# Kernel tuning notes

Measured on AMD Instinct MI355X. Metric: run time of the kernel, lower is better.

The kernel has to match this reference:

```python
import jax, jax.numpy as jnp
import numpy as np

B, T, D, H, O = 1024, 2048, 13, 128, 2


def setup_inputs() -> dict:
    key = jax.random.key(0)
    k1, k2, k3, k4 = jax.random.split(key, 4)
    xs = jax.random.normal(k1, (B, T, D), dtype=jnp.float32)
    # nn.Linear(in, out, bias=False) weights: [out, in]
    W_in = jax.random.normal(k2, (H, D), dtype=jnp.float32) / np.sqrt(D).astype(np.float32)
    W_h = jax.random.normal(k3, (H, H), dtype=jnp.float32) / np.sqrt(H).astype(np.float32)
    W_out = jax.random.normal(k4, (O, H), dtype=jnp.float32) / np.sqrt(H).astype(np.float32)
    return {"xs": xs, "W_in": W_in, "W_h": W_h, "W_out": W_out}


def reference(xs, W_in, W_h, W_out):
    # Vanilla hardtanh RNN, h0 = 0 (first step y = hardtanh(in_h(x)) == hardtanh(in_h(x) + W_h @ 0)).
    # Precompute all input projections in one big GEMM: [B, T, H]
    pre = jnp.einsum('btd,hd->bth', xs, W_in)

    def step(h, xh_t):  # h: [B, H], xh_t: [B, H]
        h = jnp.clip(xh_t + h @ W_h.T, -1.0, 1.0)  # F.hardtanh
        return h, None

    h0 = jnp.zeros((xs.shape[0], W_in.shape[0]), dtype=xs.dtype)
    hT, _ = jax.lax.scan(step, h0, jnp.swapaxes(pre, 0, 1))  # scan over time
    # Only the final hidden state per sequence is projected to the output.
    return hT @ W_out.T  # [B, O]
```

## Files before the change

kernel.cpp:

```cpp
#include <hip/hip_runtime.h>
#include <stdint.h>


#define RNN_B 1024
#define RNN_T 2048
#define RNN_D 13
#define RNN_H 128
#define RNN_O 2

#define NB 16
#define NWAVE 4
#define NTHR (NWAVE * 64)
#define ROWS 136

using f32x4 = __attribute__((ext_vector_type(4))) float;
using v8s   = __attribute__((ext_vector_type(8))) short;

__device__ __forceinline__ short f2bf(float f) {
    union { float f; uint32_t u; } c; c.f = f;
    uint32_t u = c.u + 0x7fffu + ((c.u >> 16) & 1u);
    return (short)(u >> 16);
}
__device__ __forceinline__ float bf2fs(short s) {
    union { uint32_t u; float f; } c; c.u = ((uint32_t)(uint16_t)s) << 16;
    return c.f;
}
__device__ __forceinline__ float bitf(uint32_t u) {
    union { uint32_t u; float f; } c; c.u = u; return c.f;
}
__device__ __forceinline__ uint32_t cvtpk(float a, float b) {
    uint32_t r;
    asm("v_cvt_pk_bf16_f32 %0, %1, %2" : "=v"(r) : "v"(a), "v"(b));
    return r;
}
__device__ __forceinline__ v8s pack4(uint32_t a, uint32_t b, uint32_t c, uint32_t d) {
    union { uint32_t u[4]; v8s s; } z;
    z.u[0] = a; z.u[1] = b; z.u[2] = c; z.u[3] = d; return z.s;
}
__device__ __forceinline__ float clamp1(float v) {
    return __builtin_amdgcn_fmed3f(v, -1.0f, 1.0f);
}

__device__ __forceinline__ void barrier_lgkm() {
    __builtin_amdgcn_sched_barrier(0);
    asm volatile("s_waitcnt lgkmcnt(0)" ::: "memory");
    __builtin_amdgcn_s_barrier();
    asm volatile("" ::: "memory");
    __builtin_amdgcn_sched_barrier(0);
}

#define STEP(CUR, NXT, X0, X1, X2, X3, TPF)                                      \
  do {                                                                           \
    v8s bh[4], bl[4];                                                            \
    bh[0] = *(const v8s*)&Hhi[CUR][n][g8];                                       \
    bh[1] = *(const v8s*)&Hhi[CUR][n][32 + g8];                                  \
    bh[2] = *(const v8s*)&Hhi[CUR][n][64 + g8];                                  \
    bh[3] = *(const v8s*)&Hhi[CUR][n][96 + g8];                                  \
    bl[0] = *(const v8s*)&Hlo[CUR][n][g8];                                       \
    bl[1] = *(const v8s*)&Hlo[CUR][n][32 + g8];                                  \
    bl[2] = *(const v8s*)&Hlo[CUR][n][64 + g8];                                  \
    bl[3] = *(const v8s*)&Hlo[CUR][n][96 + g8];                                  \
    float m0 = X0, m1 = X1, m2 = X2, m3 = X3;                                    \
    if (g == 3) { m1 = 0.0f; m2 = 0.0f; m3 = 0.0f; }                             \
    uint32_t xh01 = cvtpk(m0, m1), xh23 = cvtpk(m2, m3);                         \
    float q0 = m0 - bitf(xh01 << 16);                                            \
    float q1 = m1 - bitf(xh01 & 0xffff0000u);                                    \
    float q2 = m2 - bitf(xh23 << 16);                                            \
    float q3 = m3 - bitf(xh23 & 0xffff0000u);                                    \
    uint32_t xl01 = cvtpk(q0, q1), xl23 = cvtpk(q2, q3);                         \
    v8s xh = pack4(xh01, xh23, 0u, 0u);                                          \
    v8s xl = pack4(xl01, xl23, 0u, 0u);                                          \
    if ((TPF) < RNN_T) {                                                         \
      const float* xp = xrow + (size_t)(TPF) * RNN_D;                            \
      X0 = xp[d0]; X1 = xp[d1]; X2 = xp[d2]; X3 = xp[d3];                        \
    }                                                                            \
    f32x4 A1 = {0.f,0.f,0.f,0.f};                                                \
    f32x4 A2 = A1, A3 = A1, B1 = A1, B2 = A1, B3 = A1;                           \
    _Pragma("unroll")                                                            \
    for (int kt = 0; kt < 4; ++kt) {                                             \
      A1 = __builtin_amdgcn_mfma_f32_16x16x32_bf16(whiA[kt], bh[kt], A1, 0,0,0); \
      B1 = __builtin_amdgcn_mfma_f32_16x16x32_bf16(whiB[kt], bh[kt], B1, 0,0,0); \
      A2 = __builtin_amdgcn_mfma_f32_16x16x32_bf16(whiA[kt], bl[kt], A2, 0,0,0); \
      B2 = __builtin_amdgcn_mfma_f32_16x16x32_bf16(whiB[kt], bl[kt], B2, 0,0,0); \
      A3 = __builtin_amdgcn_mfma_f32_16x16x32_bf16(wloA[kt], bh[kt], A3, 0,0,0); \
      B3 = __builtin_amdgcn_mfma_f32_16x16x32_bf16(wloB[kt], bh[kt], B3, 0,0,0); \
    }                                                                            \
    A1 = __builtin_amdgcn_mfma_f32_16x16x32_bf16(whiA[4], xh, A1, 0,0,0);        \
    B1 = __builtin_amdgcn_mfma_f32_16x16x32_bf16(whiB[4], xh, B1, 0,0,0);        \
    A2 = __builtin_amdgcn_mfma_f32_16x16x32_bf16(whiA[4], xl, A2, 0,0,0);        \
    B2 = __builtin_amdgcn_mfma_f32_16x16x32_bf16(whiB[4], xl, B2, 0,0,0);        \
    A3 = __builtin_amdgcn_mfma_f32_16x16x32_bf16(wloA[4], xh, A3, 0,0,0);        \
    B3 = __builtin_amdgcn_mfma_f32_16x16x32_bf16(wloB[4], xh, B3, 0,0,0);        \
    {                                                                            \
      float v0 = clamp1(A1[0] + A2[0] + A3[0]);                                  \
      float v1 = clamp1(A1[1] + A2[1] + A3[1]);                                  \
      float v2 = clamp1(A1[2] + A2[2] + A3[2]);                                  \
      float v3 = clamp1(A1[3] + A2[3] + A3[3]);                                  \
      uint32_t h01 = cvtpk(v0, v1), h23 = cvtpk(v2, v3);                         \
      float p0 = v0 - bitf(h01 << 16);                                           \
      float p1 = v1 - bitf(h01 & 0xffff0000u);                                   \
      float p2 = v2 - bitf(h23 << 16);                                           \
      float p3 = v3 - bitf(h23 & 0xffff0000u);                                   \
      uint32_t l01 = cvtpk(p0, p1), l23 = cvtpk(p2, p3);                         \
      int2 wv; wv.x = (int)h01; wv.y = (int)h23;                                 \
      *(int2*)&Hhi[NXT][n][wbase + g8] = wv;                                     \
      wv.x = (int)l01; wv.y = (int)l23;                                          \
      *(int2*)&Hlo[NXT][n][wbase + g8] = wv;                                     \
    }                                                                            \
    {                                                                            \
      float v0 = clamp1(B1[0] + B2[0] + B3[0]);                                  \
      float v1 = clamp1(B1[1] + B2[1] + B3[1]);                                  \
      float v2 = clamp1(B1[2] + B2[2] + B3[2]);                                  \
      float v3 = clamp1(B1[3] + B2[3] + B3[3]);                                  \
      uint32_t h01 = cvtpk(v0, v1), h23 = cvtpk(v2, v3);                         \
      float p0 = v0 - bitf(h01 << 16);                                           \
      float p1 = v1 - bitf(h01 & 0xffff0000u);                                   \
      float p2 = v2 - bitf(h23 << 16);                                           \
      float p3 = v3 - bitf(h23 & 0xffff0000u);                                   \
      uint32_t l01 = cvtpk(p0, p1), l23 = cvtpk(p2, p3);                         \
      int2 wv; wv.x = (int)h01; wv.y = (int)h23;                                 \
      *(int2*)&Hhi[NXT][n][wbase + g8 + 4] = wv;                                 \
      wv.x = (int)l01; wv.y = (int)l23;                                          \
      *(int2*)&Hlo[NXT][n][wbase + g8 + 4] = wv;                                 \
    }                                                                            \
    barrier_lgkm();                                                              \
  } while (0)

__global__ __launch_bounds__(NTHR, 1) void rnn_mfma8_kernel(
    const float* __restrict__ xs,
    const float* __restrict__ W_in,
    const float* __restrict__ W_h,
    const float* __restrict__ W_out,
    float* __restrict__ out)
{
    __shared__ __align__(16) short Hhi[2][NB][ROWS];
    __shared__ __align__(16) short Hlo[2][NB][ROWS];

    const int tid  = threadIdx.x;
    const int lane = tid & 63;
    const int wid  = tid >> 6;
    const int n    = lane & 15;
    const int g    = lane >> 4;
    const int g8   = g * 8;
    const int wbase = 32 * wid;
    const int b0   = blockIdx.x * NB;

    const int d0 = (4 * g + 0 > 12) ? 12 : 4 * g + 0;
    const int d1 = (4 * g + 1 > 12) ? 12 : 4 * g + 1;
    const int d2 = (4 * g + 2 > 12) ? 12 : 4 * g + 2;
    const int d3 = (4 * g + 3 > 12) ? 12 : 4 * g + 3;

    v8s whiA[5], wloA[5], whiB[5], wloB[5];
    #pragma unroll
    for (int mi = 0; mi < 2; ++mi) {
        const int row = 16 * (wid * 2 + mi) + n;
        #pragma unroll
        for (int kt = 0; kt < 5; ++kt) {
            v8s h8, l8;
            #pragma unroll
            for (int j = 0; j < 4; ++j) {
                float w1, w2;
                if (kt < 4) {
                    w1 = W_h[row * RNN_H + 32 * kt + 4 * g + j];
                    w2 = W_h[row * RNN_H + 32 * kt + 16 + 4 * g + j];
                } else {
                    const int kx = 4 * g + j;
                    w1 = (kx < RNN_D) ? W_in[row * RNN_D + kx] : 0.0f;
                    w2 = 0.0f;
                }
                const short h1 = f2bf(w1);
                const short h2 = f2bf(w2);
                h8[j] = h1; h8[4 + j] = h2;
                l8[j] = f2bf(w1 - bf2fs(h1));
                l8[4 + j] = f2bf(w2 - bf2fs(h2));
            }
            if (mi == 0) { whiA[kt] = h8; wloA[kt] = l8; }
            else         { whiB[kt] = h8; wloB[kt] = l8; }
        }
    }

    for (int idx = tid; idx < NB * ROWS; idx += NTHR) {
        (&Hhi[0][0][0])[idx] = 0;
        (&Hlo[0][0][0])[idx] = 0;
    }

    const float* xrow = xs + (size_t)(b0 + n) * RNN_T * RNN_D;
    float xa0 = xrow[d0], xa1 = xrow[d1], xa2 = xrow[d2], xa3 = xrow[d3];
    float xb0 = xrow[RNN_D + d0], xb1 = xrow[RNN_D + d1];
    float xb2 = xrow[RNN_D + d2], xb3 = xrow[RNN_D + d3];
    __syncthreads();

    for (int t = 0; t < RNN_T; t += 2) {
        STEP(0, 1, xa0, xa1, xa2, xa3, t + 2);
        STEP(1, 0, xb0, xb1, xb2, xb3, t + 3);
    }

    __syncthreads();

    if (wid == 0 && lane < NB * RNN_O) {
        const int nn = lane & 15;
        const int o  = lane >> 4;
        float acc = 0.0f;
        for (int i = 0; i < RNN_H; ++i) {
            const int pos = 32 * (i >> 5) + 8 * ((i >> 2) & 3)
                          + 4 * ((i >> 4) & 1) + (i & 3);
            const float hv = bf2fs(Hhi[0][nn][pos]) + bf2fs(Hlo[0][nn][pos]);
            acc = fmaf(W_out[o * RNN_H + i], hv, acc);
        }
        out[(size_t)(b0 + nn) * RNN_O + o] = acc;
    }
}

extern "C" void kernel_launch(void* const* d_in, const int* in_sizes, int n_in,
                              void* d_out, int out_size, void* d_ws, size_t ws_size,
                              hipStream_t stream) {
    const float* xs    = (const float*)d_in[0];
    const float* W_in  = (const float*)d_in[1];
    const float* W_h   = (const float*)d_in[2];
    const float* W_out = (const float*)d_in[3];
    float* out = (float*)d_out;

    rnn_mfma8_kernel<<<RNN_B / NB, NTHR, 0, stream>>>(xs, W_in, W_h, W_out, out);
}
```

Baseline: 1.248 ms.

## Process two 16-sequence groups per block and issue input MFMAs first

Each block now handles 32 sequences as two independent 16-sequence groups of four waves, each group with its own LDS hidden-state buffers, and all eight waves share one barrier. The input-projection MFMAs are issued at the start of each step from zero accumulators, ahead of the recurrent MFMAs, so they can overlap the LDS reads of the hidden state. The aim is to hide the latency of the step-to-step dependency chain by interleaving two groups on one CU. In exchange the grid halves, so fewer CUs are used and each CU carries twice the MFMA work per step.

```diff
diff --git a/kernel.cpp b/kernel.cpp
--- a/kernel.cpp
+++ b/kernel.cpp
@@ -8,8 +8,8 @@
 #define RNN_H 128
 #define RNN_O 2
 
-#define NB 16
-#define NWAVE 4
+#define NB 32
+#define NWAVE 8
 #define NTHR (NWAVE * 64)
 #define ROWS 136
 
@@ -51,15 +51,17 @@
 
 #define STEP(CUR, NXT, X0, X1, X2, X3, TPF)                                      \
   do {                                                                           \
+                              \
     v8s bh[4], bl[4];                                                            \
-    bh[0] = *(const v8s*)&Hhi[CUR][n][g8];                                       \
-    bh[1] = *(const v8s*)&Hhi[CUR][n][32 + g8];                                  \
-    bh[2] = *(const v8s*)&Hhi[CUR][n][64 + g8];                                  \
-    bh[3] = *(const v8s*)&Hhi[CUR][n][96 + g8];                                  \
-    bl[0] = *(const v8s*)&Hlo[CUR][n][g8];                                       \
-    bl[1] = *(const v8s*)&Hlo[CUR][n][32 + g8];                                  \
-    bl[2] = *(const v8s*)&Hlo[CUR][n][64 + g8];                                  \
-    bl[3] = *(const v8s*)&Hlo[CUR][n][96 + g8];                                  \
+    bh[0] = *(const v8s*)&Hhi[CUR][grp][n][g8];                                  \
+    bh[1] = *(const v8s*)&Hhi[CUR][grp][n][32 + g8];                             \
+    bh[2] = *(const v8s*)&Hhi[CUR][grp][n][64 + g8];                             \
+    bh[3] = *(const v8s*)&Hhi[CUR][grp][n][96 + g8];                             \
+    bl[0] = *(const v8s*)&Hlo[CUR][grp][n][g8];                                  \
+    bl[1] = *(const v8s*)&Hlo[CUR][grp][n][32 + g8];                             \
+    bl[2] = *(const v8s*)&Hlo[CUR][grp][n][64 + g8];                             \
+    bl[3] = *(const v8s*)&Hlo[CUR][grp][n][96 + g8];                             \
+                           \
     float m0 = X0, m1 = X1, m2 = X2, m3 = X3;                                    \
     if (g == 3) { m1 = 0.0f; m2 = 0.0f; m3 = 0.0f; }                             \
     uint32_t xh01 = cvtpk(m0, m1), xh23 = cvtpk(m2, m3);                         \
@@ -70,12 +72,20 @@
     uint32_t xl01 = cvtpk(q0, q1), xl23 = cvtpk(q2, q3);                         \
     v8s xh = pack4(xh01, xh23, 0u, 0u);                                          \
     v8s xl = pack4(xl01, xl23, 0u, 0u);                                          \
+                  \
+    f32x4 Z = {0.f, 0.f, 0.f, 0.f};                                              \
+    f32x4 A1 = __builtin_amdgcn_mfma_f32_16x16x32_bf16(whiA[4], xh, Z, 0,0,0);   \
+    f32x4 B1 = __builtin_amdgcn_mfma_f32_16x16x32_bf16(whiB[4], xh, Z, 0,0,0);   \
+    f32x4 A2 = __builtin_amdgcn_mfma_f32_16x16x32_bf16(whiA[4], xl, Z, 0,0,0);   \
+    f32x4 B2 = __builtin_amdgcn_mfma_f32_16x16x32_bf16(whiB[4], xl, Z, 0,0,0);   \
+    f32x4 A3 = __builtin_amdgcn_mfma_f32_16x16x32_bf16(wloA[4], xh, Z, 0,0,0);   \
+    f32x4 B3 = __builtin_amdgcn_mfma_f32_16x16x32_bf16(wloB[4], xh, Z, 0,0,0);   \
+                                              \
     if ((TPF) < RNN_T) {                                                         \
       const float* xp = xrow + (size_t)(TPF) * RNN_D;                            \
       X0 = xp[d0]; X1 = xp[d1]; X2 = xp[d2]; X3 = xp[d3];                        \
     }                                                                            \
-    f32x4 A1 = {0.f,0.f,0.f,0.f};                                                \
-    f32x4 A2 = A1, A3 = A1, B1 = A1, B2 = A1, B3 = A1;                           \
+                                        \
     _Pragma("unroll")                                                            \
     for (int kt = 0; kt < 4; ++kt) {                                             \
       A1 = __builtin_amdgcn_mfma_f32_16x16x32_bf16(whiA[kt], bh[kt], A1, 0,0,0); \
@@ -85,12 +95,7 @@
       A3 = __builtin_amdgcn_mfma_f32_16x16x32_bf16(wloA[kt], bh[kt], A3, 0,0,0); \
       B3 = __builtin_amdgcn_mfma_f32_16x16x32_bf16(wloB[kt], bh[kt], B3, 0,0,0); \
     }                                                                            \
-    A1 = __builtin_amdgcn_mfma_f32_16x16x32_bf16(whiA[4], xh, A1, 0,0,0);        \
-    B1 = __builtin_amdgcn_mfma_f32_16x16x32_bf16(whiB[4], xh, B1, 0,0,0);        \
-    A2 = __builtin_amdgcn_mfma_f32_16x16x32_bf16(whiA[4], xl, A2, 0,0,0);        \
-    B2 = __builtin_amdgcn_mfma_f32_16x16x32_bf16(whiB[4], xl, B2, 0,0,0);        \
-    A3 = __builtin_amdgcn_mfma_f32_16x16x32_bf16(wloA[4], xh, A3, 0,0,0);        \
-    B3 = __builtin_amdgcn_mfma_f32_16x16x32_bf16(wloB[4], xh, B3, 0,0,0);        \
+                 \
     {                                                                            \
       float v0 = clamp1(A1[0] + A2[0] + A3[0]);                                  \
       float v1 = clamp1(A1[1] + A2[1] + A3[1]);                                  \
@@ -103,9 +108,9 @@
       float p3 = v3 - bitf(h23 & 0xffff0000u);                                   \
       uint32_t l01 = cvtpk(p0, p1), l23 = cvtpk(p2, p3);                         \
       int2 wv; wv.x = (int)h01; wv.y = (int)h23;                                 \
-      *(int2*)&Hhi[NXT][n][wbase + g8] = wv;                                     \
+      *(int2*)&Hhi[NXT][grp][n][wbase + g8] = wv;                                \
       wv.x = (int)l01; wv.y = (int)l23;                                          \
-      *(int2*)&Hlo[NXT][n][wbase + g8] = wv;                                     \
+      *(int2*)&Hlo[NXT][grp][n][wbase + g8] = wv;                                \
     }                                                                            \
     {                                                                            \
       float v0 = clamp1(B1[0] + B2[0] + B3[0]);                                  \
@@ -119,30 +124,32 @@
       float p3 = v3 - bitf(h23 & 0xffff0000u);                                   \
       uint32_t l01 = cvtpk(p0, p1), l23 = cvtpk(p2, p3);                         \
       int2 wv; wv.x = (int)h01; wv.y = (int)h23;                                 \
-      *(int2*)&Hhi[NXT][n][wbase + g8 + 4] = wv;                                 \
+      *(int2*)&Hhi[NXT][grp][n][wbase + g8 + 4] = wv;                            \
       wv.x = (int)l01; wv.y = (int)l23;                                          \
-      *(int2*)&Hlo[NXT][n][wbase + g8 + 4] = wv;                                 \
+      *(int2*)&Hlo[NXT][grp][n][wbase + g8 + 4] = wv;                            \
     }                                                                            \
     barrier_lgkm();                                                              \
   } while (0)
 
-__global__ __launch_bounds__(NTHR, 1) void rnn_mfma8_kernel(
+__global__ __launch_bounds__(NTHR, 1) void rnn_mfma10_kernel(
     const float* __restrict__ xs,
     const float* __restrict__ W_in,
     const float* __restrict__ W_h,
     const float* __restrict__ W_out,
     float* __restrict__ out)
 {
-    __shared__ __align__(16) short Hhi[2][NB][ROWS];
-    __shared__ __align__(16) short Hlo[2][NB][ROWS];
+    __shared__ __align__(16) short Hhi[2][2][16][ROWS];
+    __shared__ __align__(16) short Hlo[2][2][16][ROWS];
 
     const int tid  = threadIdx.x;
     const int lane = tid & 63;
     const int wid  = tid >> 6;
+    const int grp  = wid >> 2;
+    const int wg   = wid & 3;
     const int n    = lane & 15;
     const int g    = lane >> 4;
     const int g8   = g * 8;
-    const int wbase = 32 * wid;
+    const int wbase = 32 * wg;
     const int b0   = blockIdx.x * NB;
 
     const int d0 = (4 * g + 0 > 12) ? 12 : 4 * g + 0;
@@ -153,7 +160,7 @@
     v8s whiA[5], wloA[5], whiB[5], wloB[5];
     #pragma unroll
     for (int mi = 0; mi < 2; ++mi) {
-        const int row = 16 * (wid * 2 + mi) + n;
+        const int row = 16 * (wg * 2 + mi) + n;
         #pragma unroll
         for (int kt = 0; kt < 5; ++kt) {
             v8s h8, l8;
@@ -179,12 +186,12 @@
         }
     }
 
-    for (int idx = tid; idx < NB * ROWS; idx += NTHR) {
-        (&Hhi[0][0][0])[idx] = 0;
-        (&Hlo[0][0][0])[idx] = 0;
-    }
-
-    const float* xrow = xs + (size_t)(b0 + n) * RNN_T * RNN_D;
+    for (int idx = tid; idx < 2 * 16 * ROWS; idx += NTHR) {
+        (&Hhi[0][0][0][0])[idx] = 0;
+        (&Hlo[0][0][0][0])[idx] = 0;
+    }
+
+    const float* xrow = xs + (size_t)(b0 + grp * 16 + n) * RNN_T * RNN_D;
     float xa0 = xrow[d0], xa1 = xrow[d1], xa2 = xrow[d2], xa3 = xrow[d3];
     float xb0 = xrow[RNN_D + d0], xb1 = xrow[RNN_D + d1];
     float xb2 = xrow[RNN_D + d2], xb3 = xrow[RNN_D + d3];
@@ -197,17 +204,17 @@
 
     __syncthreads();
 
-    if (wid == 0 && lane < NB * RNN_O) {
+    if (wg == 0 && lane < 16 * RNN_O) {
         const int nn = lane & 15;
         const int o  = lane >> 4;
         float acc = 0.0f;
         for (int i = 0; i < RNN_H; ++i) {
             const int pos = 32 * (i >> 5) + 8 * ((i >> 2) & 3)
                           + 4 * ((i >> 4) & 1) + (i & 3);
-            const float hv = bf2fs(Hhi[0][nn][pos]) + bf2fs(Hlo[0][nn][pos]);
+            const float hv = bf2fs(Hhi[0][grp][nn][pos]) + bf2fs(Hlo[0][grp][nn][pos]);
             acc = fmaf(W_out[o * RNN_H + i], hv, acc);
         }
-        out[(size_t)(b0 + nn) * RNN_O + o] = acc;
+        out[(size_t)(b0 + grp * 16 + nn) * RNN_O + o] = acc;
     }
 }
 
@@ -220,5 +227,5 @@
     const float* W_out = (const float*)d_in[3];
     float* out = (float*)d_out;
 
-    rnn_mfma8_kernel<<<RNN_B / NB, NTHR, 0, stream>>>(xs, W_in, W_h, W_out, out);
-}
+    rnn_mfma10_kernel<<<RNN_B / NB, NTHR, 0, stream>>>(xs, W_in, W_h, W_out, out);
+}
```

Measured after the change: 1.792 ms. +43.6%, slower.
